# Kernel optimization log

Measured on AMD Instinct MI355X. Metric: run time of the kernel, lower is better.

The kernel has to match this reference:

```python
import jax, jax.numpy as jnp
import numpy as np

B, IN, NC, O, H = 256, 2048, 1000, 4096, 4  # batch, in_features, num_classes, n_decoders, hidden
NEG_SLOPE = 0.1

def setup_inputs() -> dict:
    key = jax.random.key(0)
    ks = jax.random.split(key, 7)
    s1 = 1.0 / np.sqrt(IN)
    s2 = 1.0 / np.sqrt(H)
    return {
        "x":   jax.random.normal(ks[0], (B, IN), jnp.float32),
        "fcW": jax.random.normal(ks[1], (NC, IN), jnp.float32) * s1,
        "fcb": jax.random.normal(ks[2], (NC,), jnp.float32) * s1,
        "W1":  jax.random.normal(ks[3], (O, IN, H), jnp.float32) * s1,
        "b1":  jax.random.normal(ks[4], (O, H), jnp.float32) * s1,
        "W2":  jax.random.normal(ks[5], (O, H), jnp.float32) * s2,
        "b2":  jax.random.normal(ks[6], (O,), jnp.float32) * s2,
    }

def reference(x, fcW, fcb, W1, b1, W2, b2):
    # fc head: x1 = x @ fcW^T + fcb  -> [B, NC]
    x1 = jnp.einsum("bi,ci->bc", x, fcW) + fcb
    # 4096 tiny MLPs batched into one grouped GEMM:
    # h = leaky_relu(x @ W1_o + b1_o) for each decoder o  -> [B, O, H]
    h = jnp.einsum("bi,oih->boh", x, W1) + b1
    h = jnp.where(h >= 0, h, NEG_SLOPE * h)
    # second layer (H->1) collapses to a weighted reduction -> [B, O]
    x2 = jnp.einsum("boh,oh->bo", h, W2) + b2
    return (x1, x2)
```

## Files before the change

kernel.cpp:

```cpp
#include <hip/hip_runtime.h>


typedef __bf16 bf16_t;
typedef __bf16 bf16x2v __attribute__((ext_vector_type(2)));
typedef __bf16 bf16x8 __attribute__((ext_vector_type(8)));
typedef float  f32x4  __attribute__((ext_vector_type(4)));
typedef float  f32x16 __attribute__((ext_vector_type(16)));

#define WS_REP_BYTES (1 << 20)

__device__ __forceinline__ int bslot(int n, int g) {
    return g ^ (n & 7) ^ (((n >> 3) & 3) << 1);
}

#define BARRIER() do { \
    asm volatile("s_waitcnt lgkmcnt(0)" ::: "memory"); \
    __builtin_amdgcn_s_barrier(); \
    asm volatile("" ::: "memory"); } while (0)

__global__ __launch_bounds__(256)
void pack_a(const float* __restrict__ x, char* __restrict__ ws)
{
    const int kt  = blockIdx.x & 31;
    const int rep = blockIdx.x >> 5;
    char* dst = ws + (size_t)rep * WS_REP_BYTES + (size_t)kt * 32768;
    const int tid = threadIdx.x;
    #pragma unroll
    for (int ii = 0; ii < 8; ++ii) {
        const int gi  = tid + 256 * ii;
        const int mr5 = gi >> 8, g = (gi >> 5) & 7, l = gi & 31;
        const float* sp = x + (size_t)(mr5 * 32 + l) * 2048 + kt * 64 + g * 8;
        f32x4 v0 = *(const f32x4*)sp, v1 = *(const f32x4*)(sp + 4);
        bf16x8 o;
        #pragma unroll
        for (int c = 0; c < 4; ++c) { o[c] = (bf16_t)v0[c]; o[4 + c] = (bf16_t)v1[c]; }
        *(bf16x8*)(dst + gi * 16) = o;
    }
}

__global__ __launch_bounds__(256, 4)
void fused_dual(const char* __restrict__ ws,
                const float* __restrict__ W1,
                const float* __restrict__ fcW,
                const float* __restrict__ fcb,
                const float* __restrict__ b1,
                const float* __restrict__ W2,
                const float* __restrict__ b2,
                float* __restrict__ out)
{
    __shared__ __align__(16) char lds[2][8192];

    const int tid  = threadIdx.x;
    const int lane = tid & 63, w = tid >> 6;
    const int l31  = lane & 31, half = lane >> 5;

    const int idx = blockIdx.x;
    const int wid = (idx & 7) * 132 + (idx >> 3);
    const bool is_fc = (wid >= 1024);
    const int d8 = wid >> 1, rg = wid & 1;
    const int fcI = wid - 1024;

    const char* aRep = ws + (size_t)((idx & 7) >> 1) * WS_REP_BYTES;

    int bro[4];
    #pragma unroll
    for (int ks = 0; ks < 4; ++ks)
        bro[ks] = l31 * 128 + bslot(l31, ks * 2 + half) * 16;

    if (!is_fc) {
        const int aoff = (rg * 4 + w) * 4096 + half * 512 + l31 * 16;
        const int o = (tid >> 5) & 7, kg = (tid >> 2) & 7, kp = tid & 3;
        const float* bSrc = W1 + (size_t)(d8 * 8 + o) * 8192 + (kg * 8 + kp * 2) * 4;
        int dwo[4];
        #pragma unroll
        for (int h = 0; h < 4; ++h) {
            const int n = 4 * o + h;
            dwo[h] = n * 128 + bslot(n, kg) * 16 + kp * 4;
        }

        f32x16 acc;
        #pragma unroll
        for (int r = 0; r < 16; ++r) acc[r] = 0.f;

        bf16x8 aF0[4], aF1[4];
        f32x4  bRa[4], bRb[4];

        auto B_LOAD = [&](int ss, f32x4* R) {
            const float* p = bSrc + (size_t)ss * 512;
            R[0] = *(const f32x4*)p;       R[1] = *(const f32x4*)(p + 4);
            R[2] = *(const f32x4*)(p+256); R[3] = *(const f32x4*)(p + 260);
        };
        auto B_WRITE = [&](const f32x4* R, char* lB) {
            #pragma unroll
            for (int ktl = 0; ktl < 2; ++ktl)
                #pragma unroll
                for (int h = 0; h < 4; ++h) {
                    bf16x2v v;
                    v[0] = (bf16_t)R[ktl * 2][h];
                    v[1] = (bf16_t)R[ktl * 2 + 1][h];
                    *(bf16x2v*)(lB + ktl * 4096 + dwo[h]) = v;
                }
        };
        auto A_PF = [&](int kt, bf16x8* F) {
            const char* ap = aRep + (size_t)kt * 32768 + aoff;
            #pragma unroll
            for (int ks = 0; ks < 4; ++ks)
                F[ks] = *(const bf16x8*)(ap + ks * 1024);
        };
        auto MM = [&](const bf16x8* F, const char* lB, int ktl) {
            #pragma unroll
            for (int ks = 0; ks < 4; ++ks) {
                bf16x8 bf = *(const bf16x8*)(lB + ktl * 4096 + bro[ks]);
                acc = __builtin_amdgcn_mfma_f32_32x32x16_bf16(F[ks], bf, acc, 0, 0, 0);
            }
        };

        B_LOAD(0, bRa); B_LOAD(1, bRb);
        A_PF(0, aF0);
        B_WRITE(bRa, lds[0]);
        BARRIER();

        #pragma unroll 1
        for (int ss2 = 0; ss2 < 8; ++ss2) {
            const int ss = ss2 * 2;
            {
                int sl = ss + 2; if (sl > 15) sl = 15;
                B_LOAD(sl, bRa);
                A_PF(2 * ss + 1, aF1);
                MM(aF0, lds[0], 0);
                int ka = 2 * ss + 2; if (ka > 31) ka = 31;
                A_PF(ka, aF0);
                MM(aF1, lds[0], 1);
                B_WRITE(bRb, lds[1]);
                BARRIER();
            }
            {
                int sl = ss + 3; if (sl > 15) sl = 15;
                B_LOAD(sl, bRb);
                int ka = 2 * ss + 3; if (ka > 31) ka = 31;
                A_PF(ka, aF1);
                MM(aF0, lds[1], 0);
                int kb = 2 * ss + 4; if (kb > 31) kb = 31;
                A_PF(kb, aF0);
                MM(aF1, lds[1], 1);
                B_WRITE(bRa, lds[0]);
                BARRIER();
            }
        }

        float* x2 = out + 256 * 1000;
        const int n_glob = d8 * 32 + l31;
        const float b1v = b1[n_glob], w2v = W2[n_glob];
        const float b2v = b2[n_glob >> 2];
        float* xs = (float*)lds;
        const int o8 = l31 >> 2;
        #pragma unroll
        for (int r = 0; r < 16; ++r) {
            float h = acc[r] + b1v;
            h = (h >= 0.f) ? h : 0.1f * h;
            float wv = h * w2v;
            wv += __shfl_xor(wv, 1, 64);
            wv += __shfl_xor(wv, 2, 64);
            if ((lane & 3) == 0) {
                const int row = w * 32 + (r & 3) + 8 * (r >> 2) + 4 * half;
                xs[row * 8 + o8] = wv + b2v;
            }
        }
        __syncthreads();
        {
            const int row = tid >> 1, part = tid & 1;
            f32x4 v = *(const f32x4*)(xs + row * 8 + part * 4);
            *(f32x4*)(x2 + (size_t)(rg * 128 + row) * 4096 + d8 * 8 + part * 4) = v;
        }
    } else {
        const int aoff = w * 8192 + half * 512 + l31 * 16;
        const int n = tid >> 3, kg = tid & 7;
        int c = fcI * 32 + n; if (c > 999) c = 999;
        const float* bSrc = fcW + (size_t)c * 2048 + kg * 8;
        const int fcWoff = n * 128 + bslot(n, kg) * 16;

        f32x16 acc[2];
        #pragma unroll
        for (int i = 0; i < 2; ++i)
            #pragma unroll
            for (int r = 0; r < 16; ++r) acc[i][r] = 0.f;

        bf16x8 aF[8];
        f32x4  bRa[4], bRb[4];

        auto B_LOAD = [&](int ss, f32x4* R) {
            const float* p = bSrc + (size_t)ss * 128;
            R[0] = *(const f32x4*)p;        R[1] = *(const f32x4*)(p + 4);
            R[2] = *(const f32x4*)(p + 64); R[3] = *(const f32x4*)(p + 68);
        };
        auto B_WRITE = [&](const f32x4* R, char* lB) {
            #pragma unroll
            for (int ktl = 0; ktl < 2; ++ktl) {
                bf16x8 v;
                #pragma unroll
                for (int j = 0; j < 4; ++j) {
                    v[j]     = (bf16_t)R[ktl * 2][j];
                    v[4 + j] = (bf16_t)R[ktl * 2 + 1][j];
                }
                *(bf16x8*)(lB + ktl * 4096 + fcWoff) = v;
            }
        };
        auto A_PF = [&](int kt) {
            const char* ap = aRep + (size_t)kt * 32768 + aoff;
            #pragma unroll
            for (int i = 0; i < 2; ++i)
                #pragma unroll
                for (int ks = 0; ks < 4; ++ks)
                    aF[i * 4 + ks] = *(const bf16x8*)(ap + i * 4096 + ks * 1024);
        };
        auto MM = [&](const char* lB, int ktl) {
            #pragma unroll
            for (int ks = 0; ks < 4; ++ks) {
                bf16x8 bf = *(const bf16x8*)(lB + ktl * 4096 + bro[ks]);
                #pragma unroll
                for (int i = 0; i < 2; ++i)
                    acc[i] = __builtin_amdgcn_mfma_f32_32x32x16_bf16(aF[i * 4 + ks], bf, acc[i], 0, 0, 0);
            }
        };

        B_LOAD(0, bRa); B_LOAD(1, bRb);
        B_WRITE(bRa, lds[0]);
        BARRIER();

        #pragma unroll 1
        for (int ss2 = 0; ss2 < 8; ++ss2) {
            const int ss = ss2 * 2;
            {
                int sl = ss + 2; if (sl > 15) sl = 15;
                B_LOAD(sl, bRa);
                A_PF(2 * ss);     MM(lds[0], 0);
                A_PF(2 * ss + 1); MM(lds[0], 1);
                B_WRITE(bRb, lds[1]);
                BARRIER();
            }
            {
                int sl = ss + 3; if (sl > 15) sl = 15;
                B_LOAD(sl, bRb);
                A_PF(2 * ss + 2); MM(lds[1], 0);
                A_PF(2 * ss + 3); MM(lds[1], 1);
                B_WRITE(bRa, lds[0]);
                BARRIER();
            }
        }

        const int cc = fcI * 32 + l31;
        if (cc < 1000) {
            const float bias = fcb[cc];
            #pragma unroll
            for (int i = 0; i < 2; ++i)
            #pragma unroll
            for (int r = 0; r < 16; ++r) {
                const int m = w * 64 + i * 32 + (r & 3) + 8 * (r >> 2) + 4 * half;
                out[m * 1000 + cc] = acc[i][r] + bias;
            }
        }
    }
}

extern "C" void kernel_launch(void* const* d_in, const int* in_sizes, int n_in,
                              void* d_out, int out_size, void* d_ws, size_t ws_size,
                              hipStream_t stream)
{
    (void)in_sizes; (void)n_in; (void)out_size; (void)ws_size;
    const float* x   = (const float*)d_in[0];
    const float* fcW = (const float*)d_in[1];
    const float* fcb = (const float*)d_in[2];
    const float* W1  = (const float*)d_in[3];
    const float* b1  = (const float*)d_in[4];
    const float* W2  = (const float*)d_in[5];
    const float* b2  = (const float*)d_in[6];
    char* ws = (char*)d_ws;
    pack_a<<<128, 256, 0, stream>>>(x, ws);
    fused_dual<<<1056, 256, 0, stream>>>(ws, W1, fcW, fcb, b1, W2, b2, (float*)d_out);
}
```

Measured before the change: 247.6 us.

## Deepen W1 prefetch to four register stages and fully unroll decoder K loop

Replaces the two-register-buffer B prefetch with a four-deep ring of register buffers, so global W1 loads are issued four stages ahead of their LDS write. The A fragment double buffer is dropped in favour of loading A right before each MFMA group. The 16-step K loop is fully unrolled, which removes the clamped index arithmetic. This targets global-load latency on the weight stream, at the cost of more VGPRs and possibly more exposed latency on the A loads.

```diff
diff --git a/kernel.cpp b/kernel.cpp
--- a/kernel.cpp
+++ b/kernel.cpp
@@ -82,15 +82,15 @@
         #pragma unroll
         for (int r = 0; r < 16; ++r) acc[r] = 0.f;
 
-        bf16x8 aF0[4], aF1[4];
-        f32x4  bRa[4], bRb[4];
-
-        auto B_LOAD = [&](int ss, f32x4* R) {
+        bf16x8 aF[4];
+        f32x4  bR[4][4];
+
+        auto B_LOAD = [&](int ss, f32x4 (&R)[4]) {
             const float* p = bSrc + (size_t)ss * 512;
-            R[0] = *(const f32x4*)p;       R[1] = *(const f32x4*)(p + 4);
-            R[2] = *(const f32x4*)(p+256); R[3] = *(const f32x4*)(p + 260);
-        };
-        auto B_WRITE = [&](const f32x4* R, char* lB) {
+            R[0] = *(const f32x4*)p;         R[1] = *(const f32x4*)(p + 4);
+            R[2] = *(const f32x4*)(p + 256); R[3] = *(const f32x4*)(p + 260);
+        };
+        auto B_WRITE = [&](const f32x4 (&R)[4], char* lB) {
             #pragma unroll
             for (int ktl = 0; ktl < 2; ++ktl)
                 #pragma unroll
@@ -101,13 +101,13 @@
                     *(bf16x2v*)(lB + ktl * 4096 + dwo[h]) = v;
                 }
         };
-        auto A_PF = [&](int kt, bf16x8* F) {
+        auto A_PF = [&](int kt, bf16x8 (&F)[4]) {
             const char* ap = aRep + (size_t)kt * 32768 + aoff;
             #pragma unroll
             for (int ks = 0; ks < 4; ++ks)
                 F[ks] = *(const bf16x8*)(ap + ks * 1024);
         };
-        auto MM = [&](const bf16x8* F, const char* lB, int ktl) {
+        auto MM = [&](const bf16x8 (&F)[4], const char* lB, int ktl) {
             #pragma unroll
             for (int ks = 0; ks < 4; ++ks) {
                 bf16x8 bf = *(const bf16x8*)(lB + ktl * 4096 + bro[ks]);
@@ -115,38 +115,27 @@
             }
         };
 
-        B_LOAD(0, bRa); B_LOAD(1, bRb);
-        A_PF(0, aF0);
-        B_WRITE(bRa, lds[0]);
+        B_LOAD(0, bR[0]); B_LOAD(1, bR[1]); B_LOAD(2, bR[2]); B_LOAD(3, bR[3]);
+        B_WRITE(bR[0], lds[0]);
         BARRIER();
 
-        #pragma unroll 1
-        for (int ss2 = 0; ss2 < 8; ++ss2) {
-            const int ss = ss2 * 2;
-            {
-                int sl = ss + 2; if (sl > 15) sl = 15;
-                B_LOAD(sl, bRa);
-                A_PF(2 * ss + 1, aF1);
-                MM(aF0, lds[0], 0);
-                int ka = 2 * ss + 2; if (ka > 31) ka = 31;
-                A_PF(ka, aF0);
-                MM(aF1, lds[0], 1);
-                B_WRITE(bRb, lds[1]);
-                BARRIER();
-            }
-            {
-                int sl = ss + 3; if (sl > 15) sl = 15;
-                B_LOAD(sl, bRb);
-                int ka = 2 * ss + 3; if (ka > 31) ka = 31;
-                A_PF(ka, aF1);
-                MM(aF0, lds[1], 0);
-                int kb = 2 * ss + 4; if (kb > 31) kb = 31;
-                A_PF(kb, aF0);
-                MM(aF1, lds[1], 1);
-                B_WRITE(bRa, lds[0]);
-                BARRIER();
-            }
-        }
+        #define DEC_STEP(ss, DOL, DOW) do { \
+            if (DOL) B_LOAD((ss) + 4, bR[(ss) & 3]); \
+            if (DOW) B_WRITE(bR[((ss) + 1) & 3], lds[((ss) + 1) & 1]); \
+            A_PF(2 * (ss), aF); \
+            MM(aF, lds[(ss) & 1], 0); \
+            A_PF(2 * (ss) + 1, aF); \
+            MM(aF, lds[(ss) & 1], 1); \
+            BARRIER(); \
+        } while (0)
+
+        DEC_STEP(0, 1, 1);  DEC_STEP(1, 1, 1);  DEC_STEP(2, 1, 1);
+        DEC_STEP(3, 1, 1);  DEC_STEP(4, 1, 1);  DEC_STEP(5, 1, 1);
+        DEC_STEP(6, 1, 1);  DEC_STEP(7, 1, 1);  DEC_STEP(8, 1, 1);
+        DEC_STEP(9, 1, 1);  DEC_STEP(10, 1, 1); DEC_STEP(11, 1, 1);
+        DEC_STEP(12, 0, 1); DEC_STEP(13, 0, 1); DEC_STEP(14, 0, 1);
+        DEC_STEP(15, 0, 0);
+        #undef DEC_STEP
 
         float* x2 = out + 256 * 1000;
         const int n_glob = d8 * 32 + l31;
```

New measurement: 245.1 us. About the same (-1.0%).
